# Performance work log

Measured on AMD Instinct MI355X. Metric: run time of the kernel, lower is better.

The kernel has to match this reference:

```python
import jax, jax.numpy as jnp
import numpy as np
from jax import lax

INPUT_SIZE = 64
HIDDEN = 64
LAYERS = 8
B, T = 256, 2048


def setup_inputs() -> dict:
    key = jax.random.key(0)
    ks = jax.random.split(key, 10)
    s = 1.0 / np.sqrt(HIDDEN)  # PyTorch RNN init scale U(-1/sqrt(h), 1/sqrt(h))
    u = lambda k, shape: jax.random.uniform(k, shape, jnp.float32, -s, s)
    return {
        "x": jax.random.normal(ks[0], (B, T, INPUT_SIZE), jnp.float32),
        "h_state": jnp.zeros((LAYERS, B, HIDDEN), jnp.float32),
        "W_ih0": u(ks[1], (HIDDEN, INPUT_SIZE)),        # layer-0 input weights
        "W_ih": u(ks[2], (LAYERS - 1, HIDDEN, HIDDEN)), # layers 1..7 input weights
        "W_hh": u(ks[3], (LAYERS, HIDDEN, HIDDEN)),
        "b_ih": u(ks[4], (LAYERS, HIDDEN)),
        "b_hh": u(ks[5], (LAYERS, HIDDEN)),
        "W_out": u(ks[6], (1, HIDDEN)),
        "b_out": u(ks[7], (1,)),
    }


def reference(x, h_state, W_ih0, W_ih, W_hh, b_ih, b_hh, W_out, b_out):
    # Precompute layer-0 input projection for all timesteps (one big GEMM).
    x_proj = jnp.einsum("bti,hi->bth", x, W_ih0) + b_ih[0]  # [B,T,H]
    xt = jnp.transpose(x_proj, (1, 0, 2))  # [T,B,H]

    def step(h, x_t):
        # h: [LAYERS, B, H]; one timestep of the 8-layer tanh RNN stack
        new_h = []
        inp = None
        for l in range(LAYERS):
            if l == 0:
                pre = x_t + h[0] @ W_hh[0].T + b_hh[0]
            else:
                pre = inp @ W_ih[l - 1].T + b_ih[l] + h[l] @ W_hh[l].T + b_hh[l]
            inp = jnp.tanh(pre)
            new_h.append(inp)
        return jnp.stack(new_h), inp  # carry, top-layer output

    h_final, tops = lax.scan(step, h_state, xt)  # tops: [T,B,H]
    # Batched output projection (replaces the per-timestep Python loop)
    y = jnp.transpose(tops @ W_out.T + b_out, (1, 0, 2))  # [B,T,1]
    return (y, h_final)
```

## Files before the change

kernel.cpp:

```cpp
#include <hip/hip_runtime.h>

typedef _Float16 h2 __attribute__((ext_vector_type(2)));
typedef _Float16 h8 __attribute__((ext_vector_type(8)));
typedef __fp16   g2 __attribute__((ext_vector_type(2)));
typedef __fp16   g8 __attribute__((ext_vector_type(8)));
typedef float    f32x4 __attribute__((ext_vector_type(4)));

#define TT 2048
#define HH 64
#define NL 8
#define NB 256
#define G  8
#define NCH (TT/G)
#define NI  (NCH + NL)

union GU { g8 v; g2 p[4]; h8 h; };

#define PH_BASE(l, P) (((l)*2 + (P)) * 1024)
#define CH_OFF(j, c)  ((j)*128 + (((c) ^ (j)) * 16))

__device__ __forceinline__ float tanh_fast(float v){
    float e = __expf(2.0f * v);
    float r = __builtin_amdgcn_rcpf(e + 1.0f);
    return fmaf(-2.0f, r, 1.0f);
}

__device__ __forceinline__ void barrier_lgkm_only(){
    asm volatile("" ::: "memory");
    __builtin_amdgcn_s_waitcnt(0xc07f);
    __builtin_amdgcn_s_barrier();
    asm volatile("" ::: "memory");
}


#define INTERVAL(MM, P, XC, XN) { \
    const int mm = (MM); \
    const bool act = (unsigned)(mm - wv) < (unsigned)NCH; \
    if (wv == 0){ \
        if (mm + 1 < NCH){ \
            _Pragma("unroll") \
            for (int j = 0; j < G; ++j) \
                *(_Float16*)(BB + PH_BASE(0, 1-(P)) + j*128 + (((lane>>3)^j)*16) + (lane&7)*2) = (_Float16)XC[j]; \
        } \
        if (mm + 2 < NCH){ \
            _Pragma("unroll") \
            for (int j = 0; j < G; ++j) \
                XN[j] = x[((size_t)b*TT + (mm+2)*G + j)*HH + lane]; \
        } \
    } \
    if (wv == 7 && mm >= 8){ \
        GU ha0, ha1; \
        ha0.h = *(const h8*)(BB + PH_BASE(8, P) + CH_OFF(nn&7, g)); \
        ha1.h = *(const h8*)(BB + PH_BASE(8, P) + CH_OFF(nn&7, 4+g)); \
        f32x4 ay = {0.f, 0.f, 0.f, 0.f}; \
        ay = __builtin_amdgcn_mfma_f32_16x16x32_f16(ha0.v, woutB[0].v, ay, 0, 0, 0); \
        ay = __builtin_amdgcn_mfma_f32_16x16x32_f16(ha1.v, woutB[1].v, ay, 0, 0, 0); \
        if (nn == 0 && g < 2){ \
            f32x4 st; \
            st[0] = ay[0] + bout; st[1] = ay[1] + bout; \
            st[2] = ay[2] + bout; st[3] = ay[3] + bout; \
            *(f32x4*)(yout + (size_t)b*TT + (size_t)(mm-8)*G + g*4) = st; \
        } \
    } \
    if (act){ \
         \
        GU bx0, bx1; \
        bx0.h = *(const h8*)(BB + PH_BASE(wv, P) + CH_OFF(nn&7, g)); \
        bx1.h = *(const h8*)(BB + PH_BASE(wv, P) + CH_OFF(nn&7, 4+g)); \
        f32x4 xd0 = {bs[0],bs[0],bs[0],bs[0]}, xd1 = {bs[1],bs[1],bs[1],bs[1]}; \
        f32x4 xd2 = {bs[2],bs[2],bs[2],bs[2]}, xd3 = {bs[3],bs[3],bs[3],bs[3]}; \
        xd0 = __builtin_amdgcn_mfma_f32_16x16x32_f16(bx0.v, wihA[0][0].v, xd0, 0, 0, 0); \
        xd0 = __builtin_amdgcn_mfma_f32_16x16x32_f16(bx1.v, wihA[0][1].v, xd0, 0, 0, 0); \
        xd1 = __builtin_amdgcn_mfma_f32_16x16x32_f16(bx0.v, wihA[1][0].v, xd1, 0, 0, 0); \
        xd1 = __builtin_amdgcn_mfma_f32_16x16x32_f16(bx1.v, wihA[1][1].v, xd1, 0, 0, 0); \
        xd2 = __builtin_amdgcn_mfma_f32_16x16x32_f16(bx0.v, wihA[2][0].v, xd2, 0, 0, 0); \
        xd2 = __builtin_amdgcn_mfma_f32_16x16x32_f16(bx1.v, wihA[2][1].v, xd2, 0, 0, 0); \
        xd3 = __builtin_amdgcn_mfma_f32_16x16x32_f16(bx0.v, wihA[3][0].v, xd3, 0, 0, 0); \
        xd3 = __builtin_amdgcn_mfma_f32_16x16x32_f16(bx1.v, wihA[3][1].v, xd3, 0, 0, 0); \
        if (g < 2){ \
            _Pragma("unroll") \
            for (int r = 0; r < 4; ++r){ \
                preT[wv][g*4+r][nn][0] = xd0[r]; \
                preT[wv][g*4+r][nn][1] = xd1[r]; \
                preT[wv][g*4+r][nn][2] = xd2[r]; \
                preT[wv][g*4+r][nn][3] = xd3[r]; \
            } \
        } \
         \
        _Pragma("unroll") \
        for (int j = 0; j < G; ++j){ \
            const int jx  = (j == 0) ? (G-1) : (j-1); \
            const int php = (j == 0) ? (P) : (1-(P)); \
            GU hA0, hA1; \
            hA0.h = *(const h8*)(BB + PH_BASE(wv+1, php) + CH_OFF(jx, g)); \
            hA1.h = *(const h8*)(BB + PH_BASE(wv+1, php) + CH_OFF(jx, 4+g)); \
            const f32x4 ptv = *(const f32x4*)(&preT[wv][j][nn][0]); \
            f32x4 a0 = {ptv[0], 0.f, 0.f, 0.f}; \
            f32x4 a1 = {ptv[1], 0.f, 0.f, 0.f}; \
            f32x4 a2 = {ptv[2], 0.f, 0.f, 0.f}; \
            f32x4 a3 = {ptv[3], 0.f, 0.f, 0.f}; \
            a0 = __builtin_amdgcn_mfma_f32_16x16x32_f16(hA0.v, whhB[0][0].v, a0, 0, 0, 0); \
            a0 = __builtin_amdgcn_mfma_f32_16x16x32_f16(hA1.v, whhB[0][1].v, a0, 0, 0, 0); \
            a1 = __builtin_amdgcn_mfma_f32_16x16x32_f16(hA0.v, whhB[1][0].v, a1, 0, 0, 0); \
            a1 = __builtin_amdgcn_mfma_f32_16x16x32_f16(hA1.v, whhB[1][1].v, a1, 0, 0, 0); \
            a2 = __builtin_amdgcn_mfma_f32_16x16x32_f16(hA0.v, whhB[2][0].v, a2, 0, 0, 0); \
            a2 = __builtin_amdgcn_mfma_f32_16x16x32_f16(hA1.v, whhB[2][1].v, a2, 0, 0, 0); \
            a3 = __builtin_amdgcn_mfma_f32_16x16x32_f16(hA0.v, whhB[3][0].v, a3, 0, 0, 0); \
            a3 = __builtin_amdgcn_mfma_f32_16x16x32_f16(hA1.v, whhB[3][1].v, a3, 0, 0, 0); \
            const float pa = (g & 2) ? ((g & 1) ? a3[0] : a2[0]) \
                                     : ((g & 1) ? a1[0] : a0[0]); \
            const float hn = tanh_fast(pa); \
            *(_Float16*)(BB + PH_BASE(wv+1, 1-(P)) + j*128 + (((lane>>3)^j)*16) + (lane&7)*2) = (_Float16)hn; \
            if (mm - wv == NCH-1 && j == G-1) \
                hout[((size_t)wv*NB + b)*HH + lane] = hn; \
        } \
    } \
    barrier_lgkm_only(); \
}

__global__ void __launch_bounds__(512) rnn_kernel(
    const float* __restrict__ x,
    const float* __restrict__ h_state,
    const float* __restrict__ W_ih0,
    const float* __restrict__ W_ih,
    const float* __restrict__ W_hh,
    const float* __restrict__ b_ih,
    const float* __restrict__ b_hh,
    const float* __restrict__ W_out,
    const float* __restrict__ b_out,
    float* __restrict__ out)
{
    __shared__ __attribute__((aligned(16))) _Float16 buf[(NL+1)*2*G*HH];
    __shared__ __attribute__((aligned(16))) float preT[NL][G][16][4];
    char* BB = (char*)buf;
    const int tid  = threadIdx.x;
    const int wv   = tid >> 6;
    const int lane = tid & 63;
    const int g    = lane >> 4;
    const int nn   = lane & 15;
    const size_t b = blockIdx.x;

    GU wihA[4][2], whhB[4][2];
    const float* Wi = (wv == 0) ? W_ih0 : (W_ih + (size_t)(wv-1)*HH*HH);
    const float* Wh = W_hh + (size_t)wv*HH*HH;
    #pragma unroll
    for (int t = 0; t < 4; ++t){
        #pragma unroll
        for (int kt = 0; kt < 2; ++kt){
            const float* pi = Wi + (size_t)(t*16 + nn)*HH + kt*32 + g*8;
            const float* ph = Wh + (size_t)(t*16 + nn)*HH + kt*32 + g*8;
            f32x4 i0 = *(const f32x4*)(pi), i1 = *(const f32x4*)(pi + 4);
            f32x4 h0 = *(const f32x4*)(ph), h1 = *(const f32x4*)(ph + 4);
            wihA[t][kt].p[0] = __builtin_amdgcn_cvt_pkrtz(i0[0], i0[1]);
            wihA[t][kt].p[1] = __builtin_amdgcn_cvt_pkrtz(i0[2], i0[3]);
            wihA[t][kt].p[2] = __builtin_amdgcn_cvt_pkrtz(i1[0], i1[1]);
            wihA[t][kt].p[3] = __builtin_amdgcn_cvt_pkrtz(i1[2], i1[3]);
            whhB[t][kt].p[0] = __builtin_amdgcn_cvt_pkrtz(h0[0], h0[1]);
            whhB[t][kt].p[1] = __builtin_amdgcn_cvt_pkrtz(h0[2], h0[3]);
            whhB[t][kt].p[2] = __builtin_amdgcn_cvt_pkrtz(h1[0], h1[1]);
            whhB[t][kt].p[3] = __builtin_amdgcn_cvt_pkrtz(h1[2], h1[3]);
        }
    }
    float bs[4];
    #pragma unroll
    for (int t = 0; t < 4; ++t)
        bs[t] = b_ih[wv*HH + t*16 + nn] + b_hh[wv*HH + t*16 + nn];
    float bout = b_out[0];

    GU woutB[2];
    if (wv == 7){
        #pragma unroll
        for (int kt = 0; kt < 2; ++kt)
            #pragma unroll
            for (int q = 0; q < 4; ++q)
                woutB[kt].p[q] = __builtin_amdgcn_cvt_pkrtz(
                    W_out[kt*32 + g*8 + q*2], W_out[kt*32 + g*8 + q*2 + 1]);
    }

    for (int i = tid; i < (NL+1)*2*G*HH; i += 512) buf[i] = (_Float16)0.f;
    __syncthreads();
    *(_Float16*)(BB + PH_BASE(wv+1, 1-(wv&1)) + (G-1)*128 + (((lane>>3)^(G-1))*16) + (lane&7)*2)
        = (_Float16)h_state[((size_t)wv*NB + b)*HH + lane];
    float xa[G], xb[G];
    if (wv == 0){
        #pragma unroll
        for (int j = 0; j < G; ++j){
            *(_Float16*)(BB + PH_BASE(0, 1) + j*128 + (((lane>>3)^j)*16) + (lane&7)*2)
                = (_Float16)x[((size_t)b*TT + j)*HH + lane];
            xa[j] = x[((size_t)b*TT + G + j)*HH + lane];
        }
    }
    __syncthreads();

    float* yout = out;
    float* hout = out + (size_t)NB*TT;

    for (int m2 = 0; m2 < NI; m2 += 2){
        INTERVAL(m2,     1, xa, xb)
        INTERVAL(m2 + 1, 0, xb, xa)
    }
}

extern "C" void kernel_launch(void* const* d_in, const int* in_sizes, int n_in,
                              void* d_out, int out_size, void* d_ws, size_t ws_size,
                              hipStream_t stream) {
    (void)in_sizes; (void)n_in; (void)d_ws; (void)ws_size; (void)out_size;
    const float* x       = (const float*)d_in[0];
    const float* h_state = (const float*)d_in[1];
    const float* W_ih0   = (const float*)d_in[2];
    const float* W_ih    = (const float*)d_in[3];
    const float* W_hh    = (const float*)d_in[4];
    const float* b_ih    = (const float*)d_in[5];
    const float* b_hh    = (const float*)d_in[6];
    const float* W_out   = (const float*)d_in[7];
    const float* b_out   = (const float*)d_in[8];
    float* out = (float*)d_out;

    rnn_kernel<<<dim3(NB), dim3(512), 0, stream>>>(
        x, h_state, W_ih0, W_ih, W_hh, b_ih, b_hh, W_out, b_out, out);
}
```

Measured before the change: 519.8 us.

## Shorten recurrent critical path with independent MFMAs and register-carried hidden state

The per-step recurrence now issues eight independent MFMAs from zero accumulators and sums the pairs in scalar adds, instead of chaining two dependent MFMAs per output tile seeded with the input projection. The input-projection values for all G steps are preloaded from shared memory into registers before the step loop. The previous interval's final hidden state is carried in registers (hp0/hp1), reloaded at the end of each interval rather than at the start of the next. The intent is to cut MFMA dependency latency and LDS reads on the serial critical path, at the cost of more registers and extra VALU adds.

New measurement: 518.9 us. No clear change (-0.2%).

```diff
diff --git a/kernel.cpp b/kernel.cpp
--- a/kernel.cpp
+++ b/kernel.cpp
@@ -87,30 +87,37 @@
             } \
         } \
          \
+        float pr[G]; \
+        _Pragma("unroll") \
+        for (int j = 0; j < G; ++j) pr[j] = preTf[((wv*G + j)*16 + nn)*4 + g]; \
+         \
         _Pragma("unroll") \
         for (int j = 0; j < G; ++j){ \
-            const int jx  = (j == 0) ? (G-1) : (j-1); \
-            const int php = (j == 0) ? (P) : (1-(P)); \
             GU hA0, hA1; \
-            hA0.h = *(const h8*)(BB + PH_BASE(wv+1, php) + CH_OFF(jx, g)); \
-            hA1.h = *(const h8*)(BB + PH_BASE(wv+1, php) + CH_OFF(jx, 4+g)); \
-            const f32x4 ptv = *(const f32x4*)(&preT[wv][j][nn][0]); \
-            f32x4 a0 = {ptv[0], 0.f, 0.f, 0.f}; \
-            f32x4 a1 = {ptv[1], 0.f, 0.f, 0.f}; \
-            f32x4 a2 = {ptv[2], 0.f, 0.f, 0.f}; \
-            f32x4 a3 = {ptv[3], 0.f, 0.f, 0.f}; \
-            a0 = __builtin_amdgcn_mfma_f32_16x16x32_f16(hA0.v, whhB[0][0].v, a0, 0, 0, 0); \
-            a0 = __builtin_amdgcn_mfma_f32_16x16x32_f16(hA1.v, whhB[0][1].v, a0, 0, 0, 0); \
-            a1 = __builtin_amdgcn_mfma_f32_16x16x32_f16(hA0.v, whhB[1][0].v, a1, 0, 0, 0); \
-            a1 = __builtin_amdgcn_mfma_f32_16x16x32_f16(hA1.v, whhB[1][1].v, a1, 0, 0, 0); \
-            a2 = __builtin_amdgcn_mfma_f32_16x16x32_f16(hA0.v, whhB[2][0].v, a2, 0, 0, 0); \
-            a2 = __builtin_amdgcn_mfma_f32_16x16x32_f16(hA1.v, whhB[2][1].v, a2, 0, 0, 0); \
-            a3 = __builtin_amdgcn_mfma_f32_16x16x32_f16(hA0.v, whhB[3][0].v, a3, 0, 0, 0); \
-            a3 = __builtin_amdgcn_mfma_f32_16x16x32_f16(hA1.v, whhB[3][1].v, a3, 0, 0, 0); \
-            const float pa = (g & 2) ? ((g & 1) ? a3[0] : a2[0]) \
-                                     : ((g & 1) ? a1[0] : a0[0]); \
-            const float hn = tanh_fast(pa); \
+            if (j == 0){ hA0 = hp0; hA1 = hp1; } \
+            else { \
+                hA0.h = *(const h8*)(BB + PH_BASE(wv+1, 1-(P)) + CH_OFF(j-1, g)); \
+                hA1.h = *(const h8*)(BB + PH_BASE(wv+1, 1-(P)) + CH_OFF(j-1, 4+g)); \
+            } \
+            const f32x4 zz = {0.f, 0.f, 0.f, 0.f}; \
+            f32x4 a00 = __builtin_amdgcn_mfma_f32_16x16x32_f16(hA0.v, whhB[0][0].v, zz, 0, 0, 0); \
+            f32x4 a01 = __builtin_amdgcn_mfma_f32_16x16x32_f16(hA1.v, whhB[0][1].v, zz, 0, 0, 0); \
+            f32x4 a10 = __builtin_amdgcn_mfma_f32_16x16x32_f16(hA0.v, whhB[1][0].v, zz, 0, 0, 0); \
+            f32x4 a11 = __builtin_amdgcn_mfma_f32_16x16x32_f16(hA1.v, whhB[1][1].v, zz, 0, 0, 0); \
+            f32x4 a20 = __builtin_amdgcn_mfma_f32_16x16x32_f16(hA0.v, whhB[2][0].v, zz, 0, 0, 0); \
+            f32x4 a21 = __builtin_amdgcn_mfma_f32_16x16x32_f16(hA1.v, whhB[2][1].v, zz, 0, 0, 0); \
+            f32x4 a30 = __builtin_amdgcn_mfma_f32_16x16x32_f16(hA0.v, whhB[3][0].v, zz, 0, 0, 0); \
+            f32x4 a31 = __builtin_amdgcn_mfma_f32_16x16x32_f16(hA1.v, whhB[3][1].v, zz, 0, 0, 0); \
+            const float s0 = a00[0] + a01[0], s1 = a10[0] + a11[0]; \
+            const float s2 = a20[0] + a21[0], s3 = a30[0] + a31[0]; \
+            const float pa = (g & 2) ? ((g & 1) ? s3 : s2) : ((g & 1) ? s1 : s0); \
+            const float hn = tanh_fast(pa + pr[j]); \
             *(_Float16*)(BB + PH_BASE(wv+1, 1-(P)) + j*128 + (((lane>>3)^j)*16) + (lane&7)*2) = (_Float16)hn; \
+            if (j == G-1){ \
+                 \
+                hp0.h = *(const h8*)(BB + PH_BASE(wv+1, 1-(P)) + CH_OFF(G-1, g)); \
+                hp1.h = *(const h8*)(BB + PH_BASE(wv+1, 1-(P)) + CH_OFF(G-1, 4+g)); \
+            } \
             if (mm - wv == NCH-1 && j == G-1) \
                 hout[((size_t)wv*NB + b)*HH + lane] = hn; \
         } \
@@ -133,6 +140,7 @@
     __shared__ __attribute__((aligned(16))) _Float16 buf[(NL+1)*2*G*HH];
     __shared__ __attribute__((aligned(16))) float preT[NL][G][16][4];
     char* BB = (char*)buf;
+    float* preTf = (float*)preT;
     const int tid  = threadIdx.x;
     const int wv   = tid >> 6;
     const int lane = tid & 63;
@@ -192,6 +200,10 @@
     }
     __syncthreads();
 
+    GU hp0, hp1;
+    hp0.h = *(const h8*)(BB + PH_BASE(wv+1, 1-(wv&1)) + CH_OFF(G-1, g));
+    hp1.h = *(const h8*)(BB + PH_BASE(wv+1, 1-(wv&1)) + CH_OFF(G-1, 4+g));
+
     float* yout = out;
     float* hout = out + (size_t)NB*TT;
 
```
